# Performance work log

Measured on AMD Instinct MI355X. Metric: run time of the kernel, lower is better.

## Reference

```python
import jax, jax.numpy as jnp
import numpy as np

GRID_SIZE, K, NUM_EXPERTS = 5, 3, 8
N_MLP, N_KAN = 4, 4
B, D, H, O = 4096, 512, 2048, 512


def _bspline_basis(x, grid, k):
    """Cox-de Boor recursion, vectorized. x: [B, D]; grid: [G]. Returns [B, D, G-k-1]."""
    xe = x[..., None]
    # order-0: indicator of grid interval
    b = ((grid[:-1] <= xe) & (xe < grid[1:])).astype(x.dtype)  # [B, D, G-1]
    for kk in range(1, k + 1):
        t_i = grid[: -(kk + 1)]
        t_ik = grid[kk:-1]
        t_ik1 = grid[kk + 1:]
        t_i1 = grid[1:-kk]
        left = (xe - t_i) / (t_ik - t_i) * b[..., :-1]
        right = (t_ik1 - xe) / (t_ik1 - t_i1) * b[..., 1:]
        b = left + right
    return b


def setup_inputs() -> dict:
    key = jax.random.key(0)
    ks = jax.random.split(key, 8)
    x = jax.random.normal(ks[0], (B, D), dtype=jnp.float32)
    # Router output: binary expert mask; rows with no active group fall back to expert 7
    mask = (jax.random.uniform(ks[1], (B, NUM_EXPERTS)) < 0.3).astype(jnp.float32)
    other = jnp.zeros((NUM_EXPERTS,), jnp.float32).at[7].set(1.0)
    expert_mask = jnp.where(mask.sum(axis=1, keepdims=True) == 0, other[None, :], mask)
    s_d = 1.0 / np.sqrt(D)
    s_h = 1.0 / np.sqrt(H)
    gate_w = jax.random.normal(ks[2], (D, NUM_EXPERTS), jnp.float32) * s_d
    gate_b = jnp.zeros((NUM_EXPERTS,), jnp.float32)
    mlp_w1 = jax.random.normal(ks[3], (N_MLP, D, H), jnp.float32) * s_d
    mlp_b1 = jnp.zeros((N_MLP, H), jnp.float32)
    mlp_w2 = jax.random.normal(ks[4], (N_MLP, H, O), jnp.float32) * s_h
    mlp_b2 = jnp.zeros((N_MLP, O), jnp.float32)
    kan_scaling = jnp.ones((N_KAN, D, O), jnp.float32)
    kan_coeff = jax.random.normal(ks[5], (N_KAN, D, O, GRID_SIZE + K), jnp.float32)
    return dict(x=x, expert_mask=expert_mask, gate_w=gate_w, gate_b=gate_b,
                mlp_w1=mlp_w1, mlp_b1=mlp_b1, mlp_w2=mlp_w2, mlp_b2=mlp_b2,
                kan_scaling=kan_scaling, kan_coeff=kan_coeff)


def reference(x, expert_mask, gate_w, gate_b, mlp_w1, mlp_b1, mlp_w2, mlp_b2,
              kan_scaling, kan_coeff):
    # gate softmax + router mask + renormalize
    gate = jax.nn.softmax(x @ gate_w + gate_b, axis=1)          # [B, E]
    masked = gate * expert_mask
    w = masked / (masked.sum(axis=1, keepdims=True) + 1e-9)      # [B, E]

    # MLP experts (eval mode -> dropout is identity)
    h = jax.nn.relu(jnp.einsum('bd,edh->ebh', x, mlp_w1) + mlp_b1[:, None, :])
    mlp_out = jnp.einsum('ebh,eho->ebo', h, mlp_w2) + mlp_b2[:, None, :]  # [4, B, O]

    # KAN experts: uniform grid extended by k knots each side (spacing 2/grid_size)
    hg = 2.0 / GRID_SIZE
    grid = jnp.arange(GRID_SIZE + 2 * K + 1, dtype=x.dtype) * hg - (1.0 + K * hg)
    basis = _bspline_basis(x, grid, K)                           # [B, D, 8]
    ceff = kan_coeff * kan_scaling[..., None]                    # [4, D, O, 8]
    kan_out = jnp.einsum('big,eiog->ebo', basis, ceff)           # [4, B, O]

    expert_outputs = jnp.concatenate([mlp_out, kan_out], axis=0)  # [8, B, O]
    out = jnp.einsum('ebo,be->bo', expert_outputs, w)             # [B, O]
    return out, expert_mask, w
```

## Files before the change

### kernel.cpp

```cpp
#include <hip/hip_runtime.h>

typedef __attribute__((ext_vector_type(4))) float f32x4;
typedef __attribute__((ext_vector_type(8))) __bf16 bf16x8;
typedef __attribute__((ext_vector_type(4))) unsigned short u16x4;
typedef __attribute__((ext_vector_type(8))) unsigned short u16x8;

#define NB 4096
#define ND 512
#define NH 2048
#define NO 512

__device__ __forceinline__ unsigned short f2bf(float f) {
  unsigned int u = __float_as_uint(f);
  u += 0x7fffu + ((u >> 16) & 1u);
  return (unsigned short)(u >> 16);
}
__device__ __forceinline__ float bf2f(unsigned short u) {
  return __uint_as_float(((unsigned int)u) << 16);
}
__device__ __forceinline__ void gload_lds16(const void* g, void* l) {
  __builtin_amdgcn_global_load_lds(
      (const __attribute__((address_space(1))) unsigned int*)g,
      (__attribute__((address_space(3))) unsigned int*)l, 16, 0, 0);
}

__global__ void gate_kernel(const float* __restrict__ x, const float* __restrict__ emask,
                            const float* __restrict__ gw, const float* __restrict__ gb,
                            float* __restrict__ w_out, float* __restrict__ mask_out) {
  int b = blockIdx.x;
  int lane = threadIdx.x;
  float l8[8] = {0,0,0,0,0,0,0,0};
  const float* xr = x + (size_t)b * ND;
  for (int d = lane; d < ND; d += 64) {
    float xv = xr[d];
    const float* g = gw + d * 8;
#pragma unroll
    for (int e = 0; e < 8; ++e) l8[e] = fmaf(xv, g[e], l8[e]);
  }
#pragma unroll
  for (int off = 32; off > 0; off >>= 1) {
#pragma unroll
    for (int e = 0; e < 8; ++e) l8[e] += __shfl_xor(l8[e], off);
  }
  float m = -1e30f;
#pragma unroll
  for (int e = 0; e < 8; ++e) { l8[e] += gb[e]; m = fmaxf(m, l8[e]); }
  float s = 0.f, p[8];
#pragma unroll
  for (int e = 0; e < 8; ++e) { p[e] = expf(l8[e] - m); s += p[e]; }
  float inv = 1.f / s;
  float mk[8], me[8], ms = 0.f;
#pragma unroll
  for (int e = 0; e < 8; ++e) {
    mk[e] = emask[(size_t)b * 8 + e];
    me[e] = p[e] * inv * mk[e];
    ms += me[e];
  }
  float winv = 1.f / (ms + 1e-9f);
  if (lane == 0) {
#pragma unroll
    for (int e = 0; e < 8; ++e) {
      w_out[(size_t)b * 8 + e] = me[e] * winv;
      mask_out[(size_t)b * 8 + e] = mk[e];
    }
  }
}

__global__ void cast_x_kernel(const float* __restrict__ x, unsigned short* __restrict__ xb) {
  size_t i = ((size_t)blockIdx.x * 256 + threadIdx.x) * 4;
  f32x4 v = *(const f32x4*)(x + i);
  u16x4 r;
#pragma unroll
  for (int j = 0; j < 4; ++j) r[j] = f2bf(v[j]);
  *(u16x4*)(xb + i) = r;
}

__global__ void basis_kernel(const float* __restrict__ x, unsigned short* __restrict__ bas) {
  size_t t = (size_t)blockIdx.x * 256 + threadIdx.x;
  float xv = x[t];
  const float hg = 0.4f;
  float tt[12];
#pragma unroll
  for (int j = 0; j < 12; ++j) tt[j] = -2.2f + hg * (float)j;
  float b0[11];
#pragma unroll
  for (int j = 0; j < 11; ++j) b0[j] = (tt[j] <= xv && xv < tt[j + 1]) ? 1.f : 0.f;
  float b1[10], b2[9], b3[8];
#pragma unroll
  for (int j = 0; j < 10; ++j) b1[j] = ((xv - tt[j]) * b0[j] + (tt[j + 2] - xv) * b0[j + 1]) * (1.f / (1.f * hg));
#pragma unroll
  for (int j = 0; j < 9; ++j)  b2[j] = ((xv - tt[j]) * b1[j] + (tt[j + 3] - xv) * b1[j + 1]) * (1.f / (2.f * hg));
#pragma unroll
  for (int j = 0; j < 8; ++j)  b3[j] = ((xv - tt[j]) * b2[j] + (tt[j + 4] - xv) * b2[j + 1]) * (1.f / (3.f * hg));
  u16x8 r;
#pragma unroll
  for (int j = 0; j < 8; ++j) r[j] = f2bf(b3[j]);
  *(u16x8*)(bas + t * 8) = r;
}

__global__ void transpose_cast(const float* __restrict__ in, unsigned short* __restrict__ outp,
                               int R, int Cc) {
  __shared__ float tile[32][33];
  int e = blockIdx.z;
  int c0 = blockIdx.x * 32, r0 = blockIdx.y * 32;
  int tx = threadIdx.x & 31, ty = threadIdx.x >> 5;
  const float* ine = in + (size_t)e * R * Cc;
  unsigned short* oute = outp + (size_t)e * R * Cc;
#pragma unroll
  for (int j = 0; j < 32; j += 8)
    tile[ty + j][tx] = ine[(size_t)(r0 + ty + j) * Cc + (c0 + tx)];
  __syncthreads();
#pragma unroll
  for (int j = 0; j < 32; j += 8)
    oute[(size_t)(c0 + ty + j) * R + (r0 + tx)] = f2bf(tile[tx][ty + j]);
}

__global__ void make_cefft(const float* __restrict__ coeff, const float* __restrict__ scal,
                           unsigned short* __restrict__ outp) {
  size_t t = (size_t)blockIdx.x * 256 + threadIdx.x;
  int i = (int)(t & 511);
  int o = (int)((t >> 9) & 511);
  int e = (int)(t >> 18);
  size_t io = ((size_t)e * 512 + i) * 512 + o;
  const f32x4* cp = (const f32x4*)(coeff + io * 8);
  f32x4 c0 = cp[0], c1 = cp[1];
  float s = scal[io];
  u16x8 r;
#pragma unroll
  for (int j = 0; j < 4; ++j) r[j] = f2bf(c0[j] * s);
#pragma unroll
  for (int j = 0; j < 4; ++j) r[4 + j] = f2bf(c1[j] * s);
  *(u16x8*)(outp + ((size_t)e * 512 + o) * 4096 + (size_t)i * 8) = r;
}

template <int MODE>
__global__ __launch_bounds__(512, 2) void gemm_bt(
    const unsigned short* __restrict__ A, size_t strideAe, int lda,
    const unsigned short* __restrict__ Bm, size_t strideBe, int ldb,
    const float* __restrict__ bias, int strideBiasE,
    unsigned short* __restrict__ C, size_t strideCe, int ldc, int K) {
  __shared__ __align__(16) char lsA[3 * 32768];
  __shared__ __align__(16) char lsB[3 * 16384];
  const int tid = threadIdx.x;
  const int lane = tid & 63, wid = tid >> 6;
  const int wr = wid >> 1, wc = wid & 1;
  const int brow = blockIdx.y * 256, bcol = blockIdx.x * 128;
  const int e = blockIdx.z;
  const unsigned short* Ae = A + (size_t)e * strideAe;
  const unsigned short* Be = Bm + (size_t)e * strideBe;
  const int NT = K >> 6;

  const int fr = lane & 15, fc = lane >> 4;
  const int swz = fr & 7;
  const int sR = tid >> 3, ssc = tid & 7;

  auto issueA = [&](int buf, int t2, int q) {
    int R = q * 64 + sR;
    gload_lds16(Ae + (size_t)(brow + R) * lda + (size_t)(t2 * 64 + ((ssc ^ (R & 7)) << 3)),
                lsA + buf * 32768 + q * 8192 + tid * 16);
  };
  auto issueB = [&](int buf, int t2, int q) {
    int R = q * 64 + sR;
    gload_lds16(Be + (size_t)(bcol + R) * ldb + (size_t)(t2 * 64 + ((ssc ^ (R & 7)) << 3)),
                lsB + buf * 16384 + q * 8192 + tid * 16);
  };

  f32x4 acc[4][4] = {};

  issueA(0, 0, 0); issueA(0, 0, 1); issueA(0, 0, 2); issueA(0, 0, 3);
  issueB(0, 0, 0); issueB(0, 0, 1);
  issueA(1, 1, 0); issueA(1, 1, 1); issueA(1, 1, 2); issueA(1, 1, 3);
  issueB(1, 1, 0); issueB(1, 1, 1);
  asm volatile("s_waitcnt vmcnt(6)" ::: "memory");
  __builtin_amdgcn_s_barrier();

  int bi = 0;
  for (int t = 0; t < NT; ++t) {
    char* bA = lsA + bi * 32768;
    char* bB = lsB + bi * 16384;
    int pb = (bi == 0) ? 2 : bi - 1;
    const bool pf = (t + 2 < NT);

    bf16x8 af[4], bfrag[4];
#pragma unroll
    for (int i = 0; i < 4; ++i) {
      int ra = wr * 64 + i * 16 + fr;
      af[i] = *(const bf16x8*)(bA + ra * 128 + ((fc ^ swz) << 4));
      int rb = wc * 64 + i * 16 + fr;
      bfrag[i] = *(const bf16x8*)(bB + rb * 128 + ((fc ^ swz) << 4));
    }
    if (pf) { issueA(pb, t + 2, 0); issueA(pb, t + 2, 1); issueA(pb, t + 2, 2); }
    __builtin_amdgcn_s_barrier();
    asm volatile("s_waitcnt lgkmcnt(0)" ::: "memory");
    __builtin_amdgcn_sched_barrier(0);
    __builtin_amdgcn_s_setprio(1);
#pragma unroll
    for (int mi = 0; mi < 4; ++mi)
#pragma unroll
      for (int ni = 0; ni < 4; ++ni)
        acc[mi][ni] = __builtin_amdgcn_mfma_f32_16x16x32_bf16(af[mi], bfrag[ni], acc[mi][ni], 0, 0, 0);
    __builtin_amdgcn_s_setprio(0);
    __builtin_amdgcn_s_barrier();

#pragma unroll
    for (int i = 0; i < 4; ++i) {
      int ra = wr * 64 + i * 16 + fr;
      af[i] = *(const bf16x8*)(bA + ra * 128 + (((4 + fc) ^ swz) << 4));
      int rb = wc * 64 + i * 16 + fr;
      bfrag[i] = *(const bf16x8*)(bB + rb * 128 + (((4 + fc) ^ swz) << 4));
    }
    if (pf) { issueA(pb, t + 2, 3); issueB(pb, t + 2, 0); issueB(pb, t + 2, 1); }
    __builtin_amdgcn_s_barrier();
    asm volatile("s_waitcnt lgkmcnt(0)" ::: "memory");
    __builtin_amdgcn_sched_barrier(0);
    __builtin_amdgcn_s_setprio(1);
#pragma unroll
    for (int mi = 0; mi < 4; ++mi)
#pragma unroll
      for (int ni = 0; ni < 4; ++ni)
        acc[mi][ni] = __builtin_amdgcn_mfma_f32_16x16x32_bf16(af[mi], bfrag[ni], acc[mi][ni], 0, 0, 0);
    __builtin_amdgcn_s_setprio(0);
    if (pf) asm volatile("s_waitcnt vmcnt(6)" ::: "memory");
    else    asm volatile("s_waitcnt vmcnt(0)" ::: "memory");
    __builtin_amdgcn_s_barrier();

    bi = (bi == 2) ? 0 : bi + 1;
  }

  unsigned short* Ce = C + (size_t)e * strideCe;
#pragma unroll
  for (int ni = 0; ni < 4; ++ni) {
    int col = bcol + wc * 64 + ni * 16 + fr;
    float bv = 0.f;
    if constexpr (MODE != 2) bv = bias[e * strideBiasE + col];
#pragma unroll
    for (int mi = 0; mi < 4; ++mi) {
      int row0 = brow + wr * 64 + mi * 16 + (fc << 2);
#pragma unroll
      for (int j = 0; j < 4; ++j) {
        float v = acc[mi][ni][j] + bv;
        if constexpr (MODE == 0) v = fmaxf(v, 0.f);
        Ce[(size_t)(row0 + j) * ldc + col] = f2bf(v);
      }
    }
  }
}

__global__ void combine_kernel(const unsigned short* __restrict__ eo,
                               const float* __restrict__ w, float* __restrict__ out) {
  int b = blockIdx.x;
  int o = threadIdx.x * 4;
  float wv[8];
#pragma unroll
  for (int e = 0; e < 8; ++e) wv[e] = w[(size_t)b * 8 + e];
  f32x4 acc = {0.f, 0.f, 0.f, 0.f};
#pragma unroll
  for (int e = 0; e < 8; ++e) {
    u16x4 u = *(const u16x4*)(eo + ((size_t)e * NB + b) * NO + o);
#pragma unroll
    for (int j = 0; j < 4; ++j) acc[j] = fmaf(wv[e], bf2f(u[j]), acc[j]);
  }
  *(f32x4*)(out + (size_t)b * NO + o) = acc;
}

extern "C" void kernel_launch(void* const* d_in, const int* in_sizes, int n_in,
                              void* d_out, int out_size, void* d_ws, size_t ws_size,
                              hipStream_t stream) {
  (void)in_sizes; (void)n_in; (void)out_size; (void)ws_size;
  const float* x      = (const float*)d_in[0];
  const float* emask  = (const float*)d_in[1];
  const float* gate_w = (const float*)d_in[2];
  const float* gate_b = (const float*)d_in[3];
  const float* mlp_w1 = (const float*)d_in[4];
  const float* mlp_b1 = (const float*)d_in[5];
  const float* mlp_w2 = (const float*)d_in[6];
  const float* mlp_b2 = (const float*)d_in[7];
  const float* kan_s  = (const float*)d_in[8];
  const float* kan_c  = (const float*)d_in[9];

  float* out = (float*)d_out;
  float* mask_out = out + (size_t)NB * NO;
  float* w_out    = mask_out + (size_t)NB * 8;

  char* ws = (char*)d_ws;
  size_t off = 0;
  auto take = [&](size_t bytes) { size_t r = off; off += (bytes + 255) & ~(size_t)255; return r; };
  unsigned short* w1t   = (unsigned short*)(ws + take((size_t)4 * NH * ND * 2));
  unsigned short* w2t   = (unsigned short*)(ws + take((size_t)4 * NO * NH * 2));
  unsigned short* cefft = (unsigned short*)(ws + take((size_t)4 * NO * (ND * 8) * 2));
  unsigned short* xbf   = (unsigned short*)(ws + take((size_t)NB * ND * 2));
  unsigned short* eo    = (unsigned short*)(ws + take((size_t)8 * NB * NO * 2));
  unsigned short* hbuf  = (unsigned short*)(ws + take((size_t)4 * NB * NH * 2));
  unsigned short* bas   = hbuf;

  gate_kernel<<<NB, 64, 0, stream>>>(x, emask, gate_w, gate_b, w_out, mask_out);
  cast_x_kernel<<<(NB * ND) / (256 * 4), 256, 0, stream>>>(x, xbf);
  transpose_cast<<<dim3(NH / 32, ND / 32, 4), 256, 0, stream>>>(mlp_w1, w1t, ND, NH);
  transpose_cast<<<dim3(NO / 32, NH / 32, 4), 256, 0, stream>>>(mlp_w2, w2t, NH, NO);
  make_cefft<<<(4 * ND * NO) / 256, 256, 0, stream>>>(kan_c, kan_s, cefft);

  gemm_bt<0><<<dim3(NH / 128, NB / 256, 4), 512, 0, stream>>>(
      xbf, 0, ND,
      w1t, (size_t)NH * ND, ND,
      mlp_b1, NH,
      hbuf, (size_t)NB * NH, NH, ND);
  gemm_bt<1><<<dim3(NO / 128, NB / 256, 4), 512, 0, stream>>>(
      hbuf, (size_t)NB * NH, NH,
      w2t, (size_t)NO * NH, NH,
      mlp_b2, NO,
      eo, (size_t)NB * NO, NO, NH);
  basis_kernel<<<(NB * ND) / 256, 256, 0, stream>>>(x, bas);
  gemm_bt<2><<<dim3(NO / 128, NB / 256, 4), 512, 0, stream>>>(
      bas, 0, ND * 8,
      cefft, (size_t)NO * (ND * 8), ND * 8,
      nullptr, 0,
      eo + (size_t)4 * NB * NO, (size_t)NB * NO, NO, ND * 8);

  combine_kernel<<<NB, NO / 4, 0, stream>>>(eo, w_out, out);
}
```

Measured before the change: 236.3 us.

## Enlarge GEMM tiles to 256x256, deepen pipeline, split-K with atomic fp32 outputs

Reworks the bf16 MFMA GEMM to use 256x256 output tiles per 512-thread block with a 5-slot, K=32 LDS ring and a prefetch distance of three stages. The second MLP GEMM and the KAN GEMM are split along K into two halves that accumulate with fp32 atomics into zeroed buffers, and the combine kernel now reads fp32. The aim is more operand reuse per tile and enough blocks to fill the device despite the larger tiles. The cost is one block per CU, extra memsets, atomic traffic, and fp32 intermediates that double the bytes the combine kernel reads.

```diff
diff --git a/kernel.cpp b/kernel.cpp
--- a/kernel.cpp
+++ b/kernel.cpp
@@ -134,62 +134,76 @@
 }
 
 template <int MODE>
-__global__ __launch_bounds__(512, 2) void gemm_bt(
+__global__ __launch_bounds__(512, 1) void gemm_bt(
     const unsigned short* __restrict__ A, size_t strideAe, int lda,
     const unsigned short* __restrict__ Bm, size_t strideBe, int ldb,
-    const float* __restrict__ bias, int strideBiasE,
-    unsigned short* __restrict__ C, size_t strideCe, int ldc, int K) {
-  __shared__ __align__(16) char lsA[3 * 32768];
-  __shared__ __align__(16) char lsB[3 * 16384];
+    const float* __restrict__ bias, int biasStride,
+    void* __restrict__ Cout, size_t strideCe, int ldc,
+    int Kspan, int zshift) {
+  __shared__ __align__(16) char ls[5 * 32768];
   const int tid = threadIdx.x;
   const int lane = tid & 63, wid = tid >> 6;
-  const int wr = wid >> 1, wc = wid & 1;
-  const int brow = blockIdx.y * 256, bcol = blockIdx.x * 128;
-  const int e = blockIdx.z;
-  const unsigned short* Ae = A + (size_t)e * strideAe;
-  const unsigned short* Be = Bm + (size_t)e * strideBe;
-  const int NT = K >> 6;
+  const int wr = wid >> 2, wc = wid & 3;
+  const int brow = blockIdx.y * 256, bcol = blockIdx.x * 256;
+  const int z = blockIdx.z;
+  const int e = z >> zshift;
+  const int half = z & ((1 << zshift) - 1);
+  const unsigned short* Ae = A + (size_t)e * strideAe + (size_t)half * Kspan;
+  const unsigned short* Be = Bm + (size_t)e * strideBe + (size_t)half * Kspan;
+  const int NT = Kspan >> 5;
 
   const int fr = lane & 15, fc = lane >> 4;
-  const int swz = fr & 7;
-  const int sR = tid >> 3, ssc = tid & 7;
-
-  auto issueA = [&](int buf, int t2, int q) {
-    int R = q * 64 + sR;
-    gload_lds16(Ae + (size_t)(brow + R) * lda + (size_t)(t2 * 64 + ((ssc ^ (R & 7)) << 3)),
-                lsA + buf * 32768 + q * 8192 + tid * 16);
+  int aoff[8], boff[4];
+#pragma unroll
+  for (int i = 0; i < 8; ++i) {
+    int ra = wr * 128 + i * 16 + fr;
+    aoff[i] = ra * 64 + ((fc ^ ((ra >> 1) & 3)) << 4);
+  }
+#pragma unroll
+  for (int n = 0; n < 4; ++n) {
+    int rb = wc * 64 + n * 16 + fr;
+    boff[n] = rb * 64 + ((fc ^ ((rb >> 1) & 3)) << 4);
+  }
+
+  const int sR = tid >> 2, ssc = tid & 3;
+  auto issueA = [&](int slot, int t) {
+#pragma unroll
+    for (int q = 0; q < 2; ++q) {
+      int R = q * 128 + sR;
+      gload_lds16(Ae + (size_t)(brow + R) * lda + (size_t)(t * 32 + ((ssc ^ ((R >> 1) & 3)) << 3)),
+                  ls + slot * 32768 + q * 8192 + tid * 16);
+    }
   };
-  auto issueB = [&](int buf, int t2, int q) {
-    int R = q * 64 + sR;
-    gload_lds16(Be + (size_t)(bcol + R) * ldb + (size_t)(t2 * 64 + ((ssc ^ (R & 7)) << 3)),
-                lsB + buf * 16384 + q * 8192 + tid * 16);
+  auto issueB = [&](int slot, int t) {
+#pragma unroll
+    for (int q = 0; q < 2; ++q) {
+      int R = q * 128 + sR;
+      gload_lds16(Be + (size_t)(bcol + R) * ldb + (size_t)(t * 32 + ((ssc ^ ((R >> 1) & 3)) << 3)),
+                  ls + slot * 32768 + 16384 + q * 8192 + tid * 16);
+    }
   };
 
-  f32x4 acc[4][4] = {};
-
-  issueA(0, 0, 0); issueA(0, 0, 1); issueA(0, 0, 2); issueA(0, 0, 3);
-  issueB(0, 0, 0); issueB(0, 0, 1);
-  issueA(1, 1, 0); issueA(1, 1, 1); issueA(1, 1, 2); issueA(1, 1, 3);
-  issueB(1, 1, 0); issueB(1, 1, 1);
-  asm volatile("s_waitcnt vmcnt(6)" ::: "memory");
+  f32x4 acc[8][4] = {};
+
+  issueA(0, 0); issueB(0, 0);
+  issueA(1, 1); issueB(1, 1);
+  issueA(2, 2); issueB(2, 2);
+  asm volatile("s_waitcnt vmcnt(8)" ::: "memory");
   __builtin_amdgcn_s_barrier();
 
-  int bi = 0;
+  int slot = 0;
   for (int t = 0; t < NT; ++t) {
-    char* bA = lsA + bi * 32768;
-    char* bB = lsB + bi * 16384;
-    int pb = (bi == 0) ? 2 : bi - 1;
-    const bool pf = (t + 2 < NT);
+    const char* sA = ls + slot * 32768;
+    const char* sB = sA + 16384;
+    const int slot3 = (slot >= 2) ? slot - 2 : slot + 3;
+    const bool pf = (t + 3 < NT);
 
     bf16x8 af[4], bfrag[4];
 #pragma unroll
-    for (int i = 0; i < 4; ++i) {
-      int ra = wr * 64 + i * 16 + fr;
-      af[i] = *(const bf16x8*)(bA + ra * 128 + ((fc ^ swz) << 4));
-      int rb = wc * 64 + i * 16 + fr;
-      bfrag[i] = *(const bf16x8*)(bB + rb * 128 + ((fc ^ swz) << 4));
-    }
-    if (pf) { issueA(pb, t + 2, 0); issueA(pb, t + 2, 1); issueA(pb, t + 2, 2); }
+    for (int i = 0; i < 4; ++i) af[i] = *(const bf16x8*)(sA + aoff[i]);
+#pragma unroll
+    for (int n = 0; n < 4; ++n) bfrag[n] = *(const bf16x8*)(sB + boff[n]);
+    if (pf) issueA(slot3, t + 3);
     __builtin_amdgcn_s_barrier();
     asm volatile("s_waitcnt lgkmcnt(0)" ::: "memory");
     __builtin_amdgcn_sched_barrier(0);
@@ -203,13 +217,8 @@
     __builtin_amdgcn_s_barrier();
 
 #pragma unroll
-    for (int i = 0; i < 4; ++i) {
-      int ra = wr * 64 + i * 16 + fr;
-      af[i] = *(const bf16x8*)(bA + ra * 128 + (((4 + fc) ^ swz) << 4));
-      int rb = wc * 64 + i * 16 + fr;
-      bfrag[i] = *(const bf16x8*)(bB + rb * 128 + (((4 + fc) ^ swz) << 4));
-    }
-    if (pf) { issueA(pb, t + 2, 3); issueB(pb, t + 2, 0); issueB(pb, t + 2, 1); }
+    for (int i = 0; i < 4; ++i) af[i] = *(const bf16x8*)(sA + aoff[4 + i]);
+    if (pf) issueB(slot3, t + 3);
     __builtin_amdgcn_s_barrier();
     asm volatile("s_waitcnt lgkmcnt(0)" ::: "memory");
     __builtin_amdgcn_sched_barrier(0);
@@ -218,35 +227,52 @@
     for (int mi = 0; mi < 4; ++mi)
 #pragma unroll
       for (int ni = 0; ni < 4; ++ni)
-        acc[mi][ni] = __builtin_amdgcn_mfma_f32_16x16x32_bf16(af[mi], bfrag[ni], acc[mi][ni], 0, 0, 0);
+        acc[4 + mi][ni] = __builtin_amdgcn_mfma_f32_16x16x32_bf16(af[mi], bfrag[ni], acc[4 + mi][ni], 0, 0, 0);
     __builtin_amdgcn_s_setprio(0);
-    if (pf) asm volatile("s_waitcnt vmcnt(6)" ::: "memory");
-    else    asm volatile("s_waitcnt vmcnt(0)" ::: "memory");
+
+    if (t + 3 < NT)      asm volatile("s_waitcnt vmcnt(8)" ::: "memory");
+    else if (t + 2 < NT) asm volatile("s_waitcnt vmcnt(4)" ::: "memory");
+    else if (t + 1 < NT) asm volatile("s_waitcnt vmcnt(0)" ::: "memory");
     __builtin_amdgcn_s_barrier();
 
-    bi = (bi == 2) ? 0 : bi + 1;
-  }
-
-  unsigned short* Ce = C + (size_t)e * strideCe;
-#pragma unroll
-  for (int ni = 0; ni < 4; ++ni) {
-    int col = bcol + wc * 64 + ni * 16 + fr;
-    float bv = 0.f;
-    if constexpr (MODE != 2) bv = bias[e * strideBiasE + col];
-#pragma unroll
-    for (int mi = 0; mi < 4; ++mi) {
-      int row0 = brow + wr * 64 + mi * 16 + (fc << 2);
-#pragma unroll
-      for (int j = 0; j < 4; ++j) {
-        float v = acc[mi][ni][j] + bv;
-        if constexpr (MODE == 0) v = fmaxf(v, 0.f);
-        Ce[(size_t)(row0 + j) * ldc + col] = f2bf(v);
+    slot = (slot == 4) ? 0 : slot + 1;
+  }
+
+  if constexpr (MODE == 0) {
+    unsigned short* Ce = (unsigned short*)Cout + (size_t)e * strideCe;
+#pragma unroll
+    for (int ni = 0; ni < 4; ++ni) {
+      int col = bcol + wc * 64 + ni * 16 + fr;
+      float bv = bias[e * biasStride + col];
+#pragma unroll
+      for (int mi = 0; mi < 8; ++mi) {
+        int row0 = brow + wr * 128 + mi * 16 + (fc << 2);
+#pragma unroll
+        for (int j = 0; j < 4; ++j) {
+          float v = fmaxf(acc[mi][ni][j] + bv, 0.f);
+          Ce[(size_t)(row0 + j) * ldc + col] = f2bf(v);
+        }
       }
     }
-  }
-}
-
-__global__ void combine_kernel(const unsigned short* __restrict__ eo,
+  } else {
+    float* Ce = (float*)Cout + (size_t)e * strideCe;
+    const bool ab = (MODE == 1) && (half == 0);
+#pragma unroll
+    for (int ni = 0; ni < 4; ++ni) {
+      int col = bcol + wc * 64 + ni * 16 + fr;
+      float bv = ab ? bias[e * biasStride + col] : 0.f;
+#pragma unroll
+      for (int mi = 0; mi < 8; ++mi) {
+        int row0 = brow + wr * 128 + mi * 16 + (fc << 2);
+#pragma unroll
+        for (int j = 0; j < 4; ++j)
+          unsafeAtomicAdd(&Ce[(size_t)(row0 + j) * ldc + col], acc[mi][ni][j] + bv);
+      }
+    }
+  }
+}
+
+__global__ void combine_kernel(const float* __restrict__ eoM, const float* __restrict__ eoK,
                                const float* __restrict__ w, float* __restrict__ out) {
   int b = blockIdx.x;
   int o = threadIdx.x * 4;
@@ -255,10 +281,16 @@
   for (int e = 0; e < 8; ++e) wv[e] = w[(size_t)b * 8 + e];
   f32x4 acc = {0.f, 0.f, 0.f, 0.f};
 #pragma unroll
-  for (int e = 0; e < 8; ++e) {
-    u16x4 u = *(const u16x4*)(eo + ((size_t)e * NB + b) * NO + o);
-#pragma unroll
-    for (int j = 0; j < 4; ++j) acc[j] = fmaf(wv[e], bf2f(u[j]), acc[j]);
+  for (int e = 0; e < 4; ++e) {
+    f32x4 v = *(const f32x4*)(eoM + ((size_t)e * NB + b) * NO + o);
+#pragma unroll
+    for (int j = 0; j < 4; ++j) acc[j] = fmaf(wv[e], v[j], acc[j]);
+  }
+#pragma unroll
+  for (int e = 0; e < 4; ++e) {
+    f32x4 v = *(const f32x4*)(eoK + ((size_t)e * NB + b) * NO + o);
+#pragma unroll
+    for (int j = 0; j < 4; ++j) acc[j] = fmaf(wv[4 + e], v[j], acc[j]);
   }
   *(f32x4*)(out + (size_t)b * NO + o) = acc;
 }
@@ -289,32 +321,35 @@
   unsigned short* w2t   = (unsigned short*)(ws + take((size_t)4 * NO * NH * 2));
   unsigned short* cefft = (unsigned short*)(ws + take((size_t)4 * NO * (ND * 8) * 2));
   unsigned short* xbf   = (unsigned short*)(ws + take((size_t)NB * ND * 2));
-  unsigned short* eo    = (unsigned short*)(ws + take((size_t)8 * NB * NO * 2));
+  float*          eoM   = (float*)(ws + take((size_t)4 * NB * NO * 4));
   unsigned short* hbuf  = (unsigned short*)(ws + take((size_t)4 * NB * NH * 2));
   unsigned short* bas   = hbuf;
+  float*          eoK   = (float*)((char*)hbuf + (size_t)2 * NB * NH * 2);
 
   gate_kernel<<<NB, 64, 0, stream>>>(x, emask, gate_w, gate_b, w_out, mask_out);
   cast_x_kernel<<<(NB * ND) / (256 * 4), 256, 0, stream>>>(x, xbf);
   transpose_cast<<<dim3(NH / 32, ND / 32, 4), 256, 0, stream>>>(mlp_w1, w1t, ND, NH);
   transpose_cast<<<dim3(NO / 32, NH / 32, 4), 256, 0, stream>>>(mlp_w2, w2t, NH, NO);
   make_cefft<<<(4 * ND * NO) / 256, 256, 0, stream>>>(kan_c, kan_s, cefft);
-
-  gemm_bt<0><<<dim3(NH / 128, NB / 256, 4), 512, 0, stream>>>(
+  hipMemsetAsync(eoM, 0, (size_t)4 * NB * NO * 4, stream);
+
+  gemm_bt<0><<<dim3(NH / 256, NB / 256, 4), 512, 0, stream>>>(
       xbf, 0, ND,
       w1t, (size_t)NH * ND, ND,
       mlp_b1, NH,
-      hbuf, (size_t)NB * NH, NH, ND);
-  gemm_bt<1><<<dim3(NO / 128, NB / 256, 4), 512, 0, stream>>>(
+      hbuf, (size_t)NB * NH, NH, ND, 0);
+  gemm_bt<1><<<dim3(NO / 256, NB / 256, 8), 512, 0, stream>>>(
       hbuf, (size_t)NB * NH, NH,
       w2t, (size_t)NO * NH, NH,
       mlp_b2, NO,
-      eo, (size_t)NB * NO, NO, NH);
+      eoM, (size_t)NB * NO, NO, NH / 2, 1);
   basis_kernel<<<(NB * ND) / 256, 256, 0, stream>>>(x, bas);
-  gemm_bt<2><<<dim3(NO / 128, NB / 256, 4), 512, 0, stream>>>(
+  hipMemsetAsync(eoK, 0, (size_t)4 * NB * NO * 4, stream);
+  gemm_bt<2><<<dim3(NO / 256, NB / 256, 8), 512, 0, stream>>>(
       bas, 0, ND * 8,
       cefft, (size_t)NO * (ND * 8), ND * 8,
       nullptr, 0,
-      eo + (size_t)4 * NB * NO, (size_t)NB * NO, NO, ND * 8);
-
-  combine_kernel<<<NB, NO / 4, 0, stream>>>(eo, w_out, out);
-}
+      eoK, (size_t)NB * NO, NO, (ND * 8) / 2, 1);
+
+  combine_kernel<<<NB, NO / 4, 0, stream>>>(eoM, eoK, w_out, out);
+}
```

After: 332.6 us. 1.41x slower.
